# Kernel optimization log

Hardware: AMD Instinct MI355X
Metric: run time of the kernel (lower is better)

The kernel has to match this reference:

```python
import jax, jax.numpy as jnp
import numpy as np


def setup_inputs() -> dict:
    key = jax.random.key(0)
    k1, k2, k3, k4, k5 = jax.random.split(key, 5)
    N, L, V = 8, 2048, 512
    E = 2 * V
    tokens = jax.random.randint(k1, (N, L, E), 0, 2, dtype=jnp.int64)
    s = 1.0 / np.sqrt(E)
    Wa_w = jax.random.uniform(k2, (E, E), jnp.float32, -s, s)
    Wa_b = jax.random.uniform(k3, (E,), jnp.float32, -s, s)
    Wb_w = jax.random.uniform(k4, (V, E), jnp.float32, -s, s)
    Wb_b = jax.random.uniform(k5, (V,), jnp.float32, -s, s)
    return {"tokens": tokens, "Wa_w": Wa_w, "Wa_b": Wa_b, "Wb_w": Wb_w, "Wb_b": Wb_b}


def reference(tokens, Wa_w, Wa_b, Wb_w, Wb_b):
    # x: [N, L, E] float embedding of binary tokens
    x = tokens.astype(jnp.float32)
    # q = Wa(x): [N, L, E] (torch Linear: x @ W^T + b)
    q = jnp.einsum("nle,fe->nlf", x, Wa_w) + Wa_b
    # scores: [N, L, L]; softmax over last dim
    scores = jnp.einsum("nlf,nmf->nlm", q, x)
    wts = jax.nn.softmax(scores, axis=-1)
    # a = wts @ x: [N, L, E]
    a = jnp.einsum("nlm,nme->nle", wts, x)
    # y = Wb(a): [N, L, V]; logits from last position
    y = jnp.einsum("nle,ve->nlv", a, Wb_w) + Wb_b
    logits = y[:, -1]  # [N, V]
    return logits
```

## Files before the change

kernel.cpp:

```cpp
#include <hip/hip_runtime.h>

#define NB 8
#define LS 2048
#define ED 1024
#define VD 512
#define CM 32
#define CH (LS / CM)
typedef unsigned long long u64;

__device__ inline float wave_reduce_sum(float v) {
    #pragma unroll
    for (int off = 32; off > 0; off >>= 1)
        v += __shfl_down(v, off, 64);
    return v;
}

__global__ __launch_bounds__(256) void k_pack_qrow(const int* __restrict__ tokens,
                                                   const float* __restrict__ Wa_w,
                                                   const float* __restrict__ Wa_b,
                                                   float* __restrict__ q_row,
                                                   u64* __restrict__ pk_g) {
    int b = blockIdx.x, t = threadIdx.x;
    int wave = t >> 6, lane = t & 63;
    if (b < 1024) {
        #pragma unroll
        for (int i = 0; i < 4; ++i) {
            int row = b * 16 + wave * 4 + i;
            const int* xr = tokens + (size_t)row * ED;
            u64* pkr = pk_g + (size_t)row * 16;
            #pragma unroll
            for (int k = 0; k < ED; k += 256) {
                int idx = k + lane * 4;
                int4 tv = *reinterpret_cast<const int4*>(xr + idx);
                u64 b0 = __ballot(tv.x != 0);
                u64 b1 = __ballot(tv.y != 0);
                u64 b2 = __ballot(tv.z != 0);
                u64 b3 = __ballot(tv.w != 0);
                u64 bb = b0;
                bb = (lane == 1) ? b1 : bb;
                bb = (lane == 2) ? b2 : bb;
                bb = (lane == 3) ? b3 : bb;
                if (lane < 4) pkr[((k >> 8) << 2) + lane] = bb;
            }
        }
    } else {
        int wid = (b - 1024) * 4 + wave;
        int n = wid >> 10, f = wid & (ED - 1);
        const int*   xrow = tokens + ((size_t)n * LS + (LS - 1)) * ED;
        const float* wrow = Wa_w + (size_t)f * ED;
        float acc = 0.f;
        #pragma unroll
        for (int k = 0; k < ED; k += 256) {
            int idx = k + lane * 4;
            int4   tv = *reinterpret_cast<const int4*>(xrow + idx);
            float4 w  = *reinterpret_cast<const float4*>(wrow + idx);
            acc += (float)tv.x * w.x + (float)tv.y * w.y
                 + (float)tv.z * w.z + (float)tv.w * w.w;
        }
        acc = wave_reduce_sum(acc);
        if (lane == 0) q_row[wid] = acc + Wa_b[f];
    }
}

__global__ __launch_bounds__(512) void k_flash(const float* __restrict__ q_row,
                                               const u64* __restrict__ pk_g,
                                               float* __restrict__ pa,
                                               float* __restrict__ mu_g,
                                               float* __restrict__ z_g) {
    int n = blockIdx.x >> 6;
    int c = blockIdx.x & (CH - 1);
    int t = threadIdx.x;
    int wave = t >> 6, lane = t & 63;

    __shared__ u64   pk[CM * 16];
    __shared__ float q_perm[ED];
    __shared__ float s_lds[CM];
    __shared__ float p_lds[CM];

    pk[t] = pk_g[((size_t)(n * LS + c * CM)) * 16 + t];
    {
        float2 qq = *reinterpret_cast<const float2*>(&q_row[n * ED + t * 2]);
        int e0 = t * 2, e1 = e0 + 1;
        q_perm[((((e0 >> 8) << 2) | (e0 & 3)) << 6) | ((e0 >> 2) & 63)] = qq.x;
        q_perm[((((e1 >> 8) << 2) | (e1 & 3)) << 6) | ((e1 >> 2) & 63)] = qq.y;
    }
    __syncthreads();

    #pragma unroll
    for (int i = 0; i < 4; ++i) {
        int m = wave + 8 * i;
        float acc = 0.f;
        #pragma unroll
        for (int w = 0; w < 16; ++w) {
            u64   word = pk[m * 16 + w];
            float qv   = q_perm[(w << 6) | lane];
            acc += ((word >> lane) & 1ull) ? qv : 0.f;
        }
        acc = wave_reduce_sum(acc);
        if (lane == 0) s_lds[m] = acc;
    }
    __syncthreads();

    if (wave == 0) {
        float s = (lane < CM) ? s_lds[lane] : -3.0e38f;
        float mx = s;
        #pragma unroll
        for (int off = 16; off > 0; off >>= 1) mx = fmaxf(mx, __shfl_xor(mx, off, 64));
        float p = (lane < CM) ? expf(s - mx) : 0.f;
        float z = p;
        #pragma unroll
        for (int off = 16; off > 0; off >>= 1) z += __shfl_xor(z, off, 64);
        if (lane < CM) p_lds[lane] = p;
        if (lane == 0) { mu_g[blockIdx.x] = mx; z_g[blockIdx.x] = z; }
    }
    __syncthreads();

    int w0  = ((t >> 8) << 2) | (t & 3);
    int bit = (t >> 2) & 63;
    float a0 = 0.f, a1 = 0.f;
    #pragma unroll 8
    for (int m = 0; m < CM; ++m) {
        float p  = p_lds[m];
        u64   lo = pk[m * 16 + w0];
        u64   hi = pk[m * 16 + w0 + 8];
        a0 += ((lo >> bit) & 1ull) ? p : 0.f;
        a1 += ((hi >> bit) & 1ull) ? p : 0.f;
    }
    float* par = pa + (size_t)blockIdx.x * ED;
    par[t]       = a0;
    par[t + 512] = a1;
}

__global__ __launch_bounds__(1024) void k_out(const float* __restrict__ pa,
                                              const float* __restrict__ mu_g,
                                              const float* __restrict__ z_g,
                                              const float* __restrict__ Wb_w,
                                              const float* __restrict__ Wb_b,
                                              float* __restrict__ out) {
    int n  = blockIdx.x >> 4;
    int vt = blockIdx.x & 15;
    int t  = threadIdx.x;
    int wave = t >> 6, lane = t & 63;
    __shared__ float coef[CH];
    __shared__ float a_lds[ED];

    if (wave == 0) {
        float m_c = mu_g[n * CH + lane];
        float mx = m_c;
        #pragma unroll
        for (int off = 32; off > 0; off >>= 1) mx = fmaxf(mx, __shfl_xor(mx, off, 64));
        float cf = expf(m_c - mx);
        float zc = z_g[n * CH + lane] * cf;
        float Z = zc;
        #pragma unroll
        for (int off = 32; off > 0; off >>= 1) Z += __shfl_xor(Z, off, 64);
        coef[lane] = cf / Z;
    }
    __syncthreads();

    float acc = 0.f;
    #pragma unroll
    for (int ci = 0; ci < CH; ++ci)
        acc += coef[ci] * pa[((size_t)(n * CH + ci)) * ED + t];
    a_lds[t] = acc;
    __syncthreads();

    #pragma unroll
    for (int i = 0; i < 2; ++i) {
        int v = vt * 32 + wave * 2 + i;
        const float* wr = Wb_w + (size_t)v * ED;
        float d = 0.f;
        #pragma unroll
        for (int k = 0; k < ED; k += 256) {
            int idx = k + lane * 4;
            float4 wv = *reinterpret_cast<const float4*>(wr + idx);
            float4 av = *reinterpret_cast<const float4*>(&a_lds[idx]);
            d += av.x * wv.x + av.y * wv.y + av.z * wv.z + av.w * wv.w;
        }
        d = wave_reduce_sum(d);
        if (lane == 0) out[n * VD + v] = d + Wb_b[v];
    }
}

extern "C" void kernel_launch(void* const* d_in, const int* in_sizes, int n_in,
                              void* d_out, int out_size, void* d_ws, size_t ws_size,
                              hipStream_t stream) {
    const int*   tokens = (const int*)  d_in[0];
    const float* Wa_w   = (const float*)d_in[1];
    const float* Wa_b   = (const float*)d_in[2];
    const float* Wb_w   = (const float*)d_in[3];
    const float* Wb_b   = (const float*)d_in[4];
    float* out = (float*)d_out;

    u64*   pk_g  = (u64*)d_ws;
    float* q_row = (float*)(pk_g + (size_t)NB * LS * 16);
    float* pa    = q_row + NB * ED;
    float* mu_g  = pa + (size_t)NB * CH * ED;
    float* z_g   = mu_g + NB * CH;

    k_pack_qrow<<<dim3(3072), dim3(256), 0, stream>>>(tokens, Wa_w, Wa_b, q_row, pk_g);
    k_flash<<<dim3(NB * CH), dim3(512), 0, stream>>>(q_row, pk_g, pa, mu_g, z_g);
    k_out<<<dim3(NB * 16), dim3(1024), 0, stream>>>(pa, mu_g, z_g, Wb_w, Wb_b, out);
}
```

Measured before the change: 32.92 us.

## Batch q-row GEMV over all sequences and double rows per pack block

The q-row projection now stages the last-position token row of all 8 sequences in shared memory, and each wave computes one output feature for all sequences at once. Each Wa_w row is therefore read once instead of eight times. The pack path also handles 32 rows per block instead of 16, which cuts the grid from 3072 to 768 blocks. The trade-offs are 32KB of LDS allocated in every block, including pack blocks that never use it (this may reduce occupancy), more registers, and fewer blocks to spread across the CUs.

```diff
diff --git a/kernel.cpp b/kernel.cpp
--- a/kernel.cpp
+++ b/kernel.cpp
@@ -20,12 +20,13 @@
                                                    const float* __restrict__ Wa_b,
                                                    float* __restrict__ q_row,
                                                    u64* __restrict__ pk_g) {
+    __shared__ int xs[NB][ED];
     int b = blockIdx.x, t = threadIdx.x;
     int wave = t >> 6, lane = t & 63;
-    if (b < 1024) {
-        #pragma unroll
-        for (int i = 0; i < 4; ++i) {
-            int row = b * 16 + wave * 4 + i;
+    if (b < 512) {
+        #pragma unroll
+        for (int i = 0; i < 8; ++i) {
+            int row = b * 32 + wave * 8 + i;
             const int* xr = tokens + (size_t)row * ED;
             u64* pkr = pk_g + (size_t)row * 16;
             #pragma unroll
@@ -44,21 +45,34 @@
             }
         }
     } else {
-        int wid = (b - 1024) * 4 + wave;
-        int n = wid >> 10, f = wid & (ED - 1);
-        const int*   xrow = tokens + ((size_t)n * LS + (LS - 1)) * ED;
+        #pragma unroll
+        for (int i = 0; i < 8; ++i) {
+            int v4 = i * 256 + t;
+            int n  = v4 >> 8;
+            int e  = (v4 & 255) * 4;
+            *reinterpret_cast<int4*>(&xs[n][e]) =
+                *reinterpret_cast<const int4*>(&tokens[((size_t)n * LS + (LS - 1)) * ED + e]);
+        }
+        __syncthreads();
+        int f = (b - 512) * 4 + wave;
         const float* wrow = Wa_w + (size_t)f * ED;
-        float acc = 0.f;
+        float acc[NB] = {0.f, 0.f, 0.f, 0.f, 0.f, 0.f, 0.f, 0.f};
         #pragma unroll
         for (int k = 0; k < ED; k += 256) {
             int idx = k + lane * 4;
-            int4   tv = *reinterpret_cast<const int4*>(xrow + idx);
-            float4 w  = *reinterpret_cast<const float4*>(wrow + idx);
-            acc += (float)tv.x * w.x + (float)tv.y * w.y
-                 + (float)tv.z * w.z + (float)tv.w * w.w;
-        }
-        acc = wave_reduce_sum(acc);
-        if (lane == 0) q_row[wid] = acc + Wa_b[f];
+            float4 w = *reinterpret_cast<const float4*>(wrow + idx);
+            #pragma unroll
+            for (int n = 0; n < NB; ++n) {
+                int4 tv = *reinterpret_cast<const int4*>(&xs[n][idx]);
+                acc[n] += (float)tv.x * w.x + (float)tv.y * w.y
+                        + (float)tv.z * w.z + (float)tv.w * w.w;
+            }
+        }
+        #pragma unroll
+        for (int n = 0; n < NB; ++n) {
+            float s = wave_reduce_sum(acc[n]);
+            if (lane == 0) q_row[n * ED + f] = s + Wa_b[f];
+        }
     }
 }
 
@@ -198,7 +212,7 @@
     float* mu_g  = pa + (size_t)NB * CH * ED;
     float* z_g   = mu_g + NB * CH;
 
-    k_pack_qrow<<<dim3(3072), dim3(256), 0, stream>>>(tokens, Wa_w, Wa_b, q_row, pk_g);
+    k_pack_qrow<<<dim3(768), dim3(256), 0, stream>>>(tokens, Wa_w, Wa_b, q_row, pk_g);
     k_flash<<<dim3(NB * CH), dim3(512), 0, stream>>>(q_row, pk_g, pa, mu_g, z_g);
     k_out<<<dim3(NB * 16), dim3(1024), 0, stream>>>(pa, mu_g, z_g, Wb_w, Wb_b, out);
 }
```

After: 34.60 us. 1.05x slower.
